# Kernel optimization log

Hardware: AMD Instinct MI355X
Metric: run time of the kernel (lower is better)

The kernel has to match this reference:

```python
import jax, jax.numpy as jnp
import numpy as np

N, IN_F, OUT_F = 8192, 512, 256
NEG_INF = -9e15
LEAKY_SLOPE = 0.25


def setup_inputs() -> dict:
    key = jax.random.key(0)
    k1, k2, k3, k4, k5, k6 = jax.random.split(key, 6)
    inp = {
        "input": jax.random.normal(k1, (N, IN_F), dtype=jnp.float32),
        "adj": jax.random.randint(k2, (N, N), 0, 2, dtype=jnp.int32),
        # learned params (xavier-normal-ish scale)
        "weights": jax.random.normal(k3, (IN_F, OUT_F), dtype=jnp.float32) * (2.0 / (IN_F + OUT_F)) ** 0.5,
        "a1": jax.random.normal(k4, (OUT_F, 1), dtype=jnp.float32) * (2.0 / (OUT_F + 1)) ** 0.5,
        "a2": jax.random.normal(k5, (OUT_F, 1), dtype=jnp.float32) * (2.0 / (OUT_F + 1)) ** 0.5,
        "bias": jax.random.uniform(k6, (OUT_F,), dtype=jnp.float32, minval=-1.0 / OUT_F ** 0.5, maxval=1.0 / OUT_F ** 0.5),
    }
    return inp


def reference(input, adj, weights, a1, a2, bias):
    # h = input @ W  : [N, out]
    h = input @ weights
    # e[i,j] = leaky_relu((h@a1)[i] + (h@a2)[j])  : [N, N] via broadcast
    e1 = h @ a1  # [N,1]
    e2 = h @ a2  # [N,1]
    e = e1 + e2.T
    e = jnp.where(e > 0, e, LEAKY_SLOPE * e)
    # mask non-edges, row softmax (dropout omitted: deterministic reference)
    scores = jnp.where(adj > 0, e, NEG_INF)
    attention = jax.nn.softmax(scores, axis=1)
    # aggregate + bias
    return attention @ h + bias
```

## Files before the change

kernel.cpp:

```cpp
#include <hip/hip_runtime.h>

typedef __attribute__((ext_vector_type(8))) short short8;
typedef __attribute__((ext_vector_type(4))) float floatx4;
typedef __attribute__((ext_vector_type(4))) unsigned int uintx4;
typedef __attribute__((ext_vector_type(2))) unsigned int uintx2;
typedef __attribute__((ext_vector_type(4))) int intx4;
typedef __attribute__((ext_vector_type(4))) unsigned short ushortx4;
typedef unsigned int u32;

#define NN 8192
#define KIN 512
#define COUT 256
#define SHIFT 16.0f

#define AS1 __attribute__((address_space(1)))
#define AS3 __attribute__((address_space(3)))

__device__ __forceinline__ void stage16(const void* g, void* l) {
  __builtin_amdgcn_global_load_lds((const AS1 u32*)g, (AS3 u32*)l, 16, 0, 0);
}

__device__ __forceinline__ unsigned int f2bf(float f) {
  unsigned int u = __float_as_uint(f);
  return (u + 0x7FFFu + ((u >> 16) & 1u)) >> 16;
}

__device__ __forceinline__ short8 pack8(const float* p) {
  uintx4 w;
  w.x = f2bf(p[0]) | (f2bf(p[1]) << 16);
  w.y = f2bf(p[2]) | (f2bf(p[3]) << 16);
  w.z = f2bf(p[4]) | (f2bf(p[5]) << 16);
  w.w = f2bf(p[6]) | (f2bf(p[7]) << 16);
  union { uintx4 u; short8 s; } cv; cv.u = w;
  return cv.s;
}

__global__ void k_cast_input(const float* __restrict__ in, ushortx4* __restrict__ out) {
  int idx = blockIdx.x * 256 + threadIdx.x;
  floatx4 v = ((const floatx4*)in)[idx];
  ushortx4 o;
  o.x = (unsigned short)f2bf(v.x);
  o.y = (unsigned short)f2bf(v.y);
  o.z = (unsigned short)f2bf(v.z);
  o.w = (unsigned short)f2bf(v.w);
  out[idx] = o;
}

__global__ void k_prep_w(const float* __restrict__ w, unsigned short* __restrict__ wt) {
  int idx = blockIdx.x * 256 + threadIdx.x;
  int k = idx >> 8, c = idx & 255;
  wt[c * KIN + k] = (unsigned short)f2bf(w[idx]);
}

__global__ __launch_bounds__(256)
void k_gemm_h(const unsigned short* __restrict__ inA, const unsigned short* __restrict__ wt,
              const float* __restrict__ a1, const float* __restrict__ a2,
              unsigned short* __restrict__ ht, float* __restrict__ e1, float* __restrict__ e2) {
  int wave = threadIdx.x >> 6;
  int lane = threadIdx.x & 63;
  int n = lane & 15, q = lane >> 4;
  int row0 = blockIdx.x * 64 + wave * 16;
  int mrow = row0 + n;

  floatx4 acc[16];
#pragma unroll
  for (int t = 0; t < 16; ++t) acc[t] = (floatx4){0.f, 0.f, 0.f, 0.f};

  for (int kc = 0; kc < KIN / 32; ++kc) {
    int k0 = kc * 32 + q * 8;
    short8 a = *(const short8*)(inA + (size_t)mrow * KIN + k0);
#pragma unroll
    for (int nt = 0; nt < 16; ++nt) {
      short8 b = *(const short8*)(wt + (size_t)(nt * 16 + n) * KIN + k0);
      acc[nt] = __builtin_amdgcn_mfma_f32_16x16x32_bf16(a, b, acc[nt], 0, 0, 0);
    }
  }

  int i0 = row0 + q * 4;
#pragma unroll
  for (int nt = 0; nt < 16; ++nt) {
    int c = nt * 16 + n;
    uintx2 pk;
    pk.x = f2bf(acc[nt][0]) | (f2bf(acc[nt][1]) << 16);
    pk.y = f2bf(acc[nt][2]) | (f2bf(acc[nt][3]) << 16);
    *(uintx2*)(ht + (size_t)c * NN + i0) = pk;
  }

  float s1[4] = {0.f, 0.f, 0.f, 0.f}, s2[4] = {0.f, 0.f, 0.f, 0.f};
#pragma unroll
  for (int nt = 0; nt < 16; ++nt) {
    float w1 = a1[nt * 16 + n];
    float w2 = a2[nt * 16 + n];
#pragma unroll
    for (int r = 0; r < 4; ++r) {
      s1[r] += acc[nt][r] * w1;
      s2[r] += acc[nt][r] * w2;
    }
  }
#pragma unroll
  for (int m = 1; m < 16; m <<= 1) {
#pragma unroll
    for (int r = 0; r < 4; ++r) {
      s1[r] += __shfl_xor(s1[r], m);
      s2[r] += __shfl_xor(s2[r], m);
    }
  }
  if (n == 0) {
#pragma unroll
    for (int r = 0; r < 4; ++r) {
      e1[i0 + r] = s1[r];
      e2[i0 + r] = s2[r];
    }
  }
}

__global__ __launch_bounds__(256, 2)
void k_attn_fused(const int* __restrict__ adj, const unsigned short* __restrict__ ht,
                  const float* __restrict__ e1, const float* __restrict__ e2,
                  float* __restrict__ opart, float* __restrict__ Dpart) {
  __shared__ __align__(16) char smem[69632];
  float* e2s = (float*)(smem + 65536);

  int b = blockIdx.x;
  int rg = b >> 3, js = b & 7;
  int wave = threadIdx.x >> 6, lane = threadIdx.x & 63;
  int n = lane & 15, q = lane >> 4;
  int rowblock = rg * 128;
  int rowbase = rowblock + wave * 32;
  int jbeg = js * 1024;

  ((floatx4*)e2s)[threadIdx.x] = *(const floatx4*)(e2 + jbeg + threadIdx.x * 4);

  float e1v0 = e1[rowbase + n];
  float e1v1 = e1[rowbase + 16 + n];

  floatx4 acc[2][16];
#pragma unroll
  for (int t = 0; t < 2; ++t)
#pragma unroll
    for (int nt = 0; nt < 16; ++nt) acc[t][nt] = (floatx4){0.f, 0.f, 0.f, 0.f};

  float d0 = 0.f, d1 = 0.f;

  auto stage = [&](int ch, int buf) {
    int j0g = jbeg + ch * 32;
    char* hbase = smem + buf * 32768;
#pragma unroll
    for (int i = 0; i < 4; ++i) {
      int seg = wave * 256 + i * 64 + lane;
      int c = seg >> 2;
      int j8 = (seg & 3) * 8;
      stage16(ht + (size_t)c * NN + j0g + j8, hbase + (size_t)(wave * 256 + i * 64) * 16);
    }
    char* abase = hbase + 16384 + wave * 4096;
    const int* aw = adj + (size_t)(rowblock + wave * 32) * NN + j0g;
#pragma unroll
    for (int i = 0; i < 4; ++i) {
      stage16(aw + (size_t)(i * 8 + (lane & 7)) * NN + (lane >> 3) * 4, abase + i * 1024);
    }
  };

  int rlo = n & 7, rhi = n >> 3;

  stage(0, 0);

  for (int ch = 0; ch < 32; ++ch) {
    int cur = ch & 1;
    if (ch < 31) {
      stage(ch + 1, cur ^ 1);
      asm volatile("s_waitcnt vmcnt(8) lgkmcnt(0)" ::: "memory");
    } else {
      asm volatile("s_waitcnt vmcnt(0) lgkmcnt(0)" ::: "memory");
    }
    asm volatile("s_barrier" ::: "memory");

    const char* ab = smem + cur * 32768 + 16384 + wave * 4096;
    intx4 a0a = *(const intx4*)(ab + rhi * 1024 + q * 256 + rlo * 16);
    intx4 a0b = *(const intx4*)(ab + rhi * 1024 + q * 256 + 128 + rlo * 16);
    intx4 a1a = *(const intx4*)(ab + 2048 + rhi * 1024 + q * 256 + rlo * 16);
    intx4 a1b = *(const intx4*)(ab + 2048 + rhi * 1024 + q * 256 + 128 + rlo * 16);

    floatx4 ea = *(const floatx4*)(e2s + ch * 32 + q * 8);
    floatx4 eb = *(const floatx4*)(e2s + ch * 32 + q * 8 + 4);
    float ev[8] = {ea.x, ea.y, ea.z, ea.w, eb.x, eb.y, eb.z, eb.w};

    float p0[8], p1[8];
#pragma unroll
    for (int jj = 0; jj < 8; ++jj) {
      int av0 = (jj < 4) ? a0a[jj] : a0b[jj - 4];
      int av1 = (jj < 4) ? a1a[jj] : a1b[jj - 4];
      float t0 = e1v0 + ev[jj];
      float t1 = e1v1 + ev[jj];
      float f0 = fmaxf(t0, 0.25f * t0);
      float f1 = fmaxf(t1, 0.25f * t1);
      float x0 = __expf(f0 - SHIFT);
      float x1 = __expf(f1 - SHIFT);
      p0[jj] = (av0 != 0) ? x0 : 0.f;
      p1[jj] = (av1 != 0) ? x1 : 0.f;
      d0 += p0[jj];
      d1 += p1[jj];
    }
    short8 af0 = pack8(p0);
    short8 af1 = pack8(p1);

    const short8* lb = (const short8*)(smem + (size_t)cur * 32768);
#pragma unroll
    for (int t = 0; t < 16; ++t) {
      short8 bf = lb[t * 64 + n * 4 + q];
      acc[0][t] = __builtin_amdgcn_mfma_f32_16x16x32_bf16(af0, bf, acc[0][t], 0, 0, 0);
      acc[1][t] = __builtin_amdgcn_mfma_f32_16x16x32_bf16(af1, bf, acc[1][t], 0, 0, 0);
    }

    asm volatile("s_waitcnt lgkmcnt(0)" ::: "memory");
    asm volatile("s_barrier" ::: "memory");
  }

  d0 += __shfl_xor(d0, 16); d0 += __shfl_xor(d0, 32);
  d1 += __shfl_xor(d1, 16); d1 += __shfl_xor(d1, 32);
  if (lane < 16) {
    Dpart[(size_t)js * NN + rowbase + lane] = d0;
    Dpart[(size_t)js * NN + rowbase + 16 + lane] = d1;
  }

  float* op = opart + (size_t)js * NN * COUT;
#pragma unroll
  for (int t2 = 0; t2 < 2; ++t2) {
#pragma unroll
    for (int nt = 0; nt < 16; ++nt) {
#pragma unroll
      for (int r = 0; r < 4; ++r) {
        int i = rowbase + t2 * 16 + q * 4 + r;
        op[(size_t)i * COUT + nt * 16 + n] = acc[t2][nt][r];
      }
    }
  }
}

__global__ void k_final_part(float* __restrict__ out, const float* __restrict__ opart,
                             const float* __restrict__ Dpart, const float* __restrict__ bias) {
  int i = blockIdx.x;
  int c = threadIdx.x;
  float s = 0.f, d = 0.f;
#pragma unroll
  for (int js = 0; js < 8; ++js) {
    s += opart[((size_t)js * NN + i) * COUT + c];
    d += Dpart[(size_t)js * NN + i];
  }
  out[(size_t)i * COUT + c] = s / fmaxf(d, 1e-37f) + bias[c];
}

__global__ __launch_bounds__(256, 2)
void k_attn_atomic(const int* __restrict__ adj, const unsigned short* __restrict__ ht,
                   const float* __restrict__ e1, const float* __restrict__ e2,
                   float* __restrict__ out_num, float* __restrict__ Dbuf) {
  int b = blockIdx.x;
  int rg = b >> 3, js = b & 7;
  int wave = threadIdx.x >> 6, lane = threadIdx.x & 63;
  int n = lane & 15, q = lane >> 4;
  int rowbase = rg * 128 + wave * 32;

  float e1v0 = e1[rowbase + n];
  float e1v1 = e1[rowbase + 16 + n];

  floatx4 acc[2][16];
#pragma unroll
  for (int t = 0; t < 2; ++t)
#pragma unroll
    for (int nt = 0; nt < 16; ++nt) acc[t][nt] = (floatx4){0.f, 0.f, 0.f, 0.f};

  float d0 = 0.f, d1 = 0.f;
  int jbeg = js * 1024;

  for (int ch = 0; ch < 32; ++ch) {
    int j0 = jbeg + ch * 32 + q * 8;
    floatx4 ea = *(const floatx4*)(e2 + j0);
    floatx4 eb = *(const floatx4*)(e2 + j0 + 4);
    float ev[8] = {ea.x, ea.y, ea.z, ea.w, eb.x, eb.y, eb.z, eb.w};

    intx4 A00 = *(const intx4*)(adj + (size_t)(rowbase + n) * NN + j0);
    intx4 A01 = *(const intx4*)(adj + (size_t)(rowbase + n) * NN + j0 + 4);
    intx4 A10 = *(const intx4*)(adj + (size_t)(rowbase + 16 + n) * NN + j0);
    intx4 A11 = *(const intx4*)(adj + (size_t)(rowbase + 16 + n) * NN + j0 + 4);

    float p0[8], p1[8];
#pragma unroll
    for (int jj = 0; jj < 8; ++jj) {
      int av0 = (jj < 4) ? A00[jj] : A01[jj - 4];
      int av1 = (jj < 4) ? A10[jj] : A11[jj - 4];
      float t0 = e1v0 + ev[jj];
      float t1 = e1v1 + ev[jj];
      float f0 = fmaxf(t0, 0.25f * t0);
      float f1 = fmaxf(t1, 0.25f * t1);
      float x0 = __expf(f0 - SHIFT);
      float x1 = __expf(f1 - SHIFT);
      p0[jj] = (av0 != 0) ? x0 : 0.f;
      p1[jj] = (av1 != 0) ? x1 : 0.f;
      d0 += p0[jj];
      d1 += p1[jj];
    }
    short8 af0 = pack8(p0);
    short8 af1 = pack8(p1);

#pragma unroll
    for (int g = 0; g < 2; ++g) {
      short8 bf[8];
#pragma unroll
      for (int t = 0; t < 8; ++t)
        bf[t] = *(const short8*)(ht + (size_t)((g * 8 + t) * 16 + n) * NN + j0);
#pragma unroll
      for (int t = 0; t < 8; ++t) {
        acc[0][g * 8 + t] = __builtin_amdgcn_mfma_f32_16x16x32_bf16(af0, bf[t], acc[0][g * 8 + t], 0, 0, 0);
        acc[1][g * 8 + t] = __builtin_amdgcn_mfma_f32_16x16x32_bf16(af1, bf[t], acc[1][g * 8 + t], 0, 0, 0);
      }
    }
  }

  d0 += __shfl_xor(d0, 16); d0 += __shfl_xor(d0, 32);
  d1 += __shfl_xor(d1, 16); d1 += __shfl_xor(d1, 32);
  if (lane < 16) {
    atomicAdd(Dbuf + rowbase + lane, d0);
    atomicAdd(Dbuf + rowbase + 16 + lane, d1);
  }

#pragma unroll
  for (int t2 = 0; t2 < 2; ++t2) {
#pragma unroll
    for (int nt = 0; nt < 16; ++nt) {
#pragma unroll
      for (int r = 0; r < 4; ++r) {
        int i = rowbase + t2 * 16 + q * 4 + r;
        atomicAdd(out_num + (size_t)i * COUT + nt * 16 + n, acc[t2][nt][r]);
      }
    }
  }
}

__global__ void k_final_atomic(float* __restrict__ out, const float* __restrict__ Dbuf,
                               const float* __restrict__ bias) {
  int idx = blockIdx.x * 256 + threadIdx.x;
  int i = idx >> 8, c = idx & 255;
  float d = fmaxf(Dbuf[i], 1e-37f);
  out[idx] = out[idx] / d + bias[c];
}

extern "C" void kernel_launch(void* const* d_in, const int* in_sizes, int n_in,
                              void* d_out, int out_size, void* d_ws, size_t ws_size,
                              hipStream_t stream) {
  const float* input   = (const float*)d_in[0];
  const int*   adj     = (const int*)d_in[1];
  const float* weights = (const float*)d_in[2];
  const float* a1      = (const float*)d_in[3];
  const float* a2      = (const float*)d_in[4];
  const float* bias    = (const float*)d_in[5];
  float* out = (float*)d_out;
  char* ws = (char*)d_ws;

  unsigned short* inA = (unsigned short*)(ws);
  unsigned short* wt  = (unsigned short*)(ws + 8388608);
  unsigned short* ht  = (unsigned short*)(ws + 8650752);
  float* e1    = (float*)(ws + 12845056);
  float* e2    = (float*)(ws + 12877824);
  float* Dpart = (float*)(ws + 12910592);
  float* opart = (float*)(ws + 13172736);
  const size_t WS_NEEDED_PART = 13172736 + (size_t)8 * NN * COUT * 4;
  float* Dbuf = Dpart;

  k_cast_input<<<4096, 256, 0, stream>>>(input, (ushortx4*)inA);
  k_prep_w<<<512, 256, 0, stream>>>(weights, wt);
  k_gemm_h<<<128, 256, 0, stream>>>(inA, wt, a1, a2, ht, e1, e2);

  if (ws_size >= WS_NEEDED_PART) {
    k_attn_fused<<<512, 256, 0, stream>>>(adj, ht, e1, e2, opart, Dpart);
    k_final_part<<<8192, 256, 0, stream>>>(out, opart, Dpart, bias);
  } else {
    hipMemsetAsync(out, 0, (size_t)NN * COUT * sizeof(float), stream);
    hipMemsetAsync(Dbuf, 0, NN * sizeof(float), stream);
    k_attn_atomic<<<512, 256, 0, stream>>>(adj, ht, e1, e2, out, Dbuf);
    k_final_atomic<<<8192, 256, 0, stream>>>(out, Dbuf, bias);
  }
}
```

Measured before the change: 453.4 us.

## Factor exp of leaky-relu into precomputed row/col products and MFMA row sums

Rewrites exp(leaky(e1+e2)-shift) as max(A1[i]*B1[j], A2[i]*B2[j]) using exp factors precomputed in the h GEMM epilogue, so the inner loop does multiplies and a max instead of per-element exp. The column factors are packed as two bf16 halves in one word. Row denominators are now computed with an extra MFMA against a ones vector instead of scalar adds, and bf16 packing uses a cheaper perm-based round. A barrier is moved so the score computation overlaps the wait. The bf16 factors and fixed shift change numerical precision and overflow behaviour.

```diff
diff --git a/kernel.cpp b/kernel.cpp
--- a/kernel.cpp
+++ b/kernel.cpp
@@ -25,12 +25,18 @@
   return (u + 0x7FFFu + ((u >> 16) & 1u)) >> 16;
 }
 
+__device__ __forceinline__ u32 pkbf(float lo, float hi) {
+  u32 a = __float_as_uint(lo) + 0x8000u;
+  u32 b = __float_as_uint(hi) + 0x8000u;
+  return __builtin_amdgcn_perm(b, a, 0x07060302u);
+}
+
 __device__ __forceinline__ short8 pack8(const float* p) {
   uintx4 w;
-  w.x = f2bf(p[0]) | (f2bf(p[1]) << 16);
-  w.y = f2bf(p[2]) | (f2bf(p[3]) << 16);
-  w.z = f2bf(p[4]) | (f2bf(p[5]) << 16);
-  w.w = f2bf(p[6]) | (f2bf(p[7]) << 16);
+  w.x = pkbf(p[0], p[1]);
+  w.y = pkbf(p[2], p[3]);
+  w.z = pkbf(p[4], p[5]);
+  w.w = pkbf(p[6], p[7]);
   union { uintx4 u; short8 s; } cv; cv.u = w;
   return cv.s;
 }
@@ -55,7 +61,8 @@
 __global__ __launch_bounds__(256)
 void k_gemm_h(const unsigned short* __restrict__ inA, const unsigned short* __restrict__ wt,
               const float* __restrict__ a1, const float* __restrict__ a2,
-              unsigned short* __restrict__ ht, float* __restrict__ e1, float* __restrict__ e2) {
+              unsigned short* __restrict__ ht, float* __restrict__ e1, float* __restrict__ e2,
+              float* __restrict__ A1, float* __restrict__ A2, u32* __restrict__ e2pk) {
   int wave = threadIdx.x >> 6;
   int lane = threadIdx.x & 63;
   int n = lane & 15, q = lane >> 4;
@@ -108,18 +115,25 @@
   if (n == 0) {
 #pragma unroll
     for (int r = 0; r < 4; ++r) {
-      e1[i0 + r] = s1[r];
-      e2[i0 + r] = s2[r];
+      float v1 = s1[r], v2 = s2[r];
+      e1[i0 + r] = v1;
+      e2[i0 + r] = v2;
+      A1[i0 + r] = __expf(v1 - 8.0f);
+      A2[i0 + r] = __expf(0.25f * v1 - 8.0f);
+      u32 b1 = f2bf(__expf(v2 - 8.0f));
+      u32 b2 = f2bf(__expf(0.25f * v2 - 8.0f));
+      e2pk[i0 + r] = (b1 << 16) | b2;
     }
   }
 }
 
 __global__ __launch_bounds__(256, 2)
 void k_attn_fused(const int* __restrict__ adj, const unsigned short* __restrict__ ht,
-                  const float* __restrict__ e1, const float* __restrict__ e2,
+                  const float* __restrict__ A1, const float* __restrict__ A2,
+                  const u32* __restrict__ e2pk,
                   float* __restrict__ opart, float* __restrict__ Dpart) {
   __shared__ __align__(16) char smem[69632];
-  float* e2s = (float*)(smem + 65536);
+  u32* e2s = (u32*)(smem + 65536);
 
   int b = blockIdx.x;
   int rg = b >> 3, js = b & 7;
@@ -129,18 +143,23 @@
   int rowbase = rowblock + wave * 32;
   int jbeg = js * 1024;
 
-  ((floatx4*)e2s)[threadIdx.x] = *(const floatx4*)(e2 + jbeg + threadIdx.x * 4);
-
-  float e1v0 = e1[rowbase + n];
-  float e1v1 = e1[rowbase + 16 + n];
+  ((uintx4*)e2s)[threadIdx.x] = *(const uintx4*)(e2pk + jbeg + threadIdx.x * 4);
+
+  float A1v0 = A1[rowbase + n],      A2v0 = A2[rowbase + n];
+  float A1v1 = A1[rowbase + 16 + n], A2v1 = A2[rowbase + 16 + n];
 
   floatx4 acc[2][16];
-#pragma unroll
-  for (int t = 0; t < 2; ++t)
+  floatx4 accd[2];
+#pragma unroll
+  for (int t = 0; t < 2; ++t) {
+    accd[t] = (floatx4){0.f, 0.f, 0.f, 0.f};
 #pragma unroll
     for (int nt = 0; nt < 16; ++nt) acc[t][nt] = (floatx4){0.f, 0.f, 0.f, 0.f};
-
-  float d0 = 0.f, d1 = 0.f;
+  }
+
+  union { uintx4 u; short8 s; } onesu;
+  onesu.u = (uintx4){0x3F803F80u, 0x3F803F80u, 0x3F803F80u, 0x3F803F80u};
+  short8 ones = onesu.s;
 
   auto stage = [&](int ch, int buf) {
     int j0g = jbeg + ch * 32;
@@ -163,16 +182,17 @@
   int rlo = n & 7, rhi = n >> 3;
 
   stage(0, 0);
+  asm volatile("s_waitcnt lgkmcnt(0)" ::: "memory");
+  asm volatile("s_barrier" ::: "memory");
 
   for (int ch = 0; ch < 32; ++ch) {
     int cur = ch & 1;
     if (ch < 31) {
       stage(ch + 1, cur ^ 1);
-      asm volatile("s_waitcnt vmcnt(8) lgkmcnt(0)" ::: "memory");
+      asm volatile("s_waitcnt vmcnt(8)" ::: "memory");
     } else {
-      asm volatile("s_waitcnt vmcnt(0) lgkmcnt(0)" ::: "memory");
-    }
-    asm volatile("s_barrier" ::: "memory");
+      asm volatile("s_waitcnt vmcnt(0)" ::: "memory");
+    }
 
     const char* ab = smem + cur * 32768 + 16384 + wave * 4096;
     intx4 a0a = *(const intx4*)(ab + rhi * 1024 + q * 256 + rlo * 16);
@@ -180,28 +200,28 @@
     intx4 a1a = *(const intx4*)(ab + 2048 + rhi * 1024 + q * 256 + rlo * 16);
     intx4 a1b = *(const intx4*)(ab + 2048 + rhi * 1024 + q * 256 + 128 + rlo * 16);
 
-    floatx4 ea = *(const floatx4*)(e2s + ch * 32 + q * 8);
-    floatx4 eb = *(const floatx4*)(e2s + ch * 32 + q * 8 + 4);
-    float ev[8] = {ea.x, ea.y, ea.z, ea.w, eb.x, eb.y, eb.z, eb.w};
+    uintx4 ba = *(const uintx4*)(e2s + ch * 32 + q * 8);
+    uintx4 bb = *(const uintx4*)(e2s + ch * 32 + q * 8 + 4);
+    u32 bw[8] = {ba.x, ba.y, ba.z, ba.w, bb.x, bb.y, bb.z, bb.w};
 
     float p0[8], p1[8];
 #pragma unroll
     for (int jj = 0; jj < 8; ++jj) {
       int av0 = (jj < 4) ? a0a[jj] : a0b[jj - 4];
       int av1 = (jj < 4) ? a1a[jj] : a1b[jj - 4];
-      float t0 = e1v0 + ev[jj];
-      float t1 = e1v1 + ev[jj];
-      float f0 = fmaxf(t0, 0.25f * t0);
-      float f1 = fmaxf(t1, 0.25f * t1);
-      float x0 = __expf(f0 - SHIFT);
-      float x1 = __expf(f1 - SHIFT);
-      p0[jj] = (av0 != 0) ? x0 : 0.f;
-      p1[jj] = (av1 != 0) ? x1 : 0.f;
-      d0 += p0[jj];
-      d1 += p1[jj];
+      float B1 = __uint_as_float(bw[jj] & 0xffff0000u);
+      float B2 = __uint_as_float(bw[jj] << 16);
+      float m10 = A1v0 * B1, m20 = A2v0 * B2;
+      float m11 = A1v1 * B1, m21 = A2v1 * B2;
+      float pm0 = fmaxf(m10, m20);
+      float pm1 = fmaxf(m11, m21);
+      p0[jj] = (av0 != 0) ? pm0 : 0.f;
+      p1[jj] = (av1 != 0) ? pm1 : 0.f;
     }
     short8 af0 = pack8(p0);
     short8 af1 = pack8(p1);
+
+    asm volatile("s_barrier" ::: "memory");
 
     const short8* lb = (const short8*)(smem + (size_t)cur * 32768);
 #pragma unroll
@@ -210,16 +230,19 @@
       acc[0][t] = __builtin_amdgcn_mfma_f32_16x16x32_bf16(af0, bf, acc[0][t], 0, 0, 0);
       acc[1][t] = __builtin_amdgcn_mfma_f32_16x16x32_bf16(af1, bf, acc[1][t], 0, 0, 0);
     }
+    accd[0] = __builtin_amdgcn_mfma_f32_16x16x32_bf16(af0, ones, accd[0], 0, 0, 0);
+    accd[1] = __builtin_amdgcn_mfma_f32_16x16x32_bf16(af1, ones, accd[1], 0, 0, 0);
 
     asm volatile("s_waitcnt lgkmcnt(0)" ::: "memory");
     asm volatile("s_barrier" ::: "memory");
   }
 
-  d0 += __shfl_xor(d0, 16); d0 += __shfl_xor(d0, 32);
-  d1 += __shfl_xor(d1, 16); d1 += __shfl_xor(d1, 32);
-  if (lane < 16) {
-    Dpart[(size_t)js * NN + rowbase + lane] = d0;
-    Dpart[(size_t)js * NN + rowbase + 16 + lane] = d1;
+  if (n == 0) {
+#pragma unroll
+    for (int t2 = 0; t2 < 2; ++t2)
+#pragma unroll
+      for (int r = 0; r < 4; ++r)
+        Dpart[(size_t)js * NN + rowbase + t2 * 16 + q * 4 + r] = accd[t2][r];
   }
 
   float* op = opart + (size_t)js * NN * COUT;
@@ -360,17 +383,20 @@
   unsigned short* ht  = (unsigned short*)(ws + 8650752);
   float* e1    = (float*)(ws + 12845056);
   float* e2    = (float*)(ws + 12877824);
-  float* Dpart = (float*)(ws + 12910592);
-  float* opart = (float*)(ws + 13172736);
-  const size_t WS_NEEDED_PART = 13172736 + (size_t)8 * NN * COUT * 4;
+  float* A1    = (float*)(ws + 12910592);
+  float* A2    = (float*)(ws + 12943360);
+  u32*   e2pk  = (u32*)  (ws + 12976128);
+  float* Dpart = (float*)(ws + 13008896);
+  float* opart = (float*)(ws + 13271040);
+  const size_t WS_NEEDED_PART = 13271040 + (size_t)8 * NN * COUT * 4;
   float* Dbuf = Dpart;
 
   k_cast_input<<<4096, 256, 0, stream>>>(input, (ushortx4*)inA);
   k_prep_w<<<512, 256, 0, stream>>>(weights, wt);
-  k_gemm_h<<<128, 256, 0, stream>>>(inA, wt, a1, a2, ht, e1, e2);
+  k_gemm_h<<<128, 256, 0, stream>>>(inA, wt, a1, a2, ht, e1, e2, A1, A2, e2pk);
 
   if (ws_size >= WS_NEEDED_PART) {
-    k_attn_fused<<<512, 256, 0, stream>>>(adj, ht, e1, e2, opart, Dpart);
+    k_attn_fused<<<512, 256, 0, stream>>>(adj, ht, A1, A2, e2pk, opart, Dpart);
     k_final_part<<<8192, 256, 0, stream>>>(out, opart, Dpart, bias);
   } else {
     hipMemsetAsync(out, 0, (size_t)NN * COUT * sizeof(float), stream);
```

Result: no change. 455.6 us (+0.5%).
